# Optimization experiments

Hardware: AMD Instinct MI355X
Metric: run time of the kernel (lower is better)

The kernel has to match this reference:

```python
import jax, jax.numpy as jnp
import numpy as np

N, E, H, HEADS, L = 10000, 64000, 128, 8, 8
D = H // HEADS
CUTOFF = 5.0
EPS = 1e-5


def _xavier(key, shape):
    lim = float(np.sqrt(6.0 / (shape[0] + shape[1])))
    return jax.random.uniform(key, shape, minval=-lim, maxval=lim, dtype=jnp.float32)


def setup_inputs() -> dict:
    key = jax.random.key(0)
    ks = jax.random.split(key, 20)
    zeros = lambda *s: jnp.zeros(s, jnp.float32)
    return {
        "x": jax.random.normal(ks[0], (N, H), jnp.float32),
        "vec": 0.1 * jax.random.normal(ks[1], (N, L, H), jnp.float32),
        "f_ij": jax.random.normal(ks[2], (E, H), jnp.float32),
        "d_ij": jax.random.normal(ks[3], (E, L), jnp.float32),
        "r_ij": jax.random.uniform(ks[4], (E,), jnp.float32, 0.0, CUTOFF),
        "edge_index": jax.random.randint(ks[5], (2, E), 0, N),
        "ln_g": jnp.ones((H,), jnp.float32), "ln_b": zeros(H),
        "vln_w": jnp.ones((H,), jnp.float32),
        "W_vec": _xavier(ks[6], (H, 3 * H)),
        "W_q": _xavier(ks[7], (H, H)), "b_q": zeros(H),
        "W_k": _xavier(ks[8], (H, H)), "b_k": zeros(H),
        "W_v": _xavier(ks[9], (H, H)), "b_v": zeros(H),
        "W_dk": _xavier(ks[10], (H, H)), "b_dk": zeros(H),
        "W_dv": _xavier(ks[11], (H, H)), "b_dv": zeros(H),
        "W_s": _xavier(ks[12], (H, 2 * H)), "b_s": zeros(2 * H),
        "W_f": _xavier(ks[13], (H, H)), "b_f": zeros(H),
        "W_src": _xavier(ks[14], (H, H)),
        "W_trg": _xavier(ks[15], (H, H)),
        "W_o": _xavier(ks[16], (H, 3 * H)), "b_o": zeros(3 * H),
    }


def _layernorm(x, g, b):
    mu = jnp.mean(x, -1, keepdims=True)
    var = jnp.mean((x - mu) ** 2, -1, keepdims=True)
    return (x - mu) * jax.lax.rsqrt(var + EPS) * g + b


def _cutoff(r):
    # CosineCutoff: 0.5*(cos(pi*r/cutoff)+1) for r < cutoff
    return 0.5 * (jnp.cos(jnp.pi * r / CUTOFF) + 1.0) * (r < CUTOFF).astype(r.dtype)


def _vec_rejection(v, d):
    # v: [E, L, H], d: [E, L]; remove the component of v along d (per channel)
    proj = jnp.einsum("elh,el->eh", v, d)
    return v - proj[:, None, :] * d[:, :, None]


def reference(x, vec, f_ij, d_ij, r_ij, edge_index, ln_g, ln_b, vln_w, W_vec,
              W_q, b_q, W_k, b_k, W_v, b_v, W_dk, b_dk, W_dv, b_dv,
              W_s, b_s, W_f, b_f, W_src, W_trg, W_o, b_o):
    src, dst = edge_index[0], edge_index[1]  # j (source), i (target)
    x = _layernorm(x, ln_g, ln_b)
    vec = vec * vln_w  # VecLayerNorm with norm_type="none": identity norm * weight

    q = (x @ W_q + b_q).reshape(N, HEADS, D)
    k = (x @ W_k + b_k).reshape(N, HEADS, D)
    v = (x @ W_v + b_v).reshape(N, HEADS, D)
    dk = jax.nn.silu(f_ij @ W_dk + b_dk).reshape(E, HEADS, D)
    dv = jax.nn.silu(f_ij @ W_dv + b_dv).reshape(E, HEADS, D)

    vec1, vec2, vec3 = jnp.split(jnp.einsum("nlh,hk->nlk", vec, W_vec), 3, axis=-1)
    vec_dot = jnp.sum(vec1 * vec2, axis=1)  # [N, H]

    # ---- message (per edge) ----
    attn = jnp.sum(q[dst] * k[src] * dk, axis=-1)          # [E, HEADS]
    attn = jax.nn.silu(attn) * _cutoff(r_ij)[:, None]
    vm = (v[src] * dv * attn[:, :, None]).reshape(E, H)    # [E, H]
    s1, s2 = jnp.split(jax.nn.silu(vm @ W_s + b_s), 2, axis=-1)
    vec_m = vec[src] * s1[:, None, :] + s2[:, None, :] * d_ij[:, :, None]  # [E, L, H]

    # ---- aggregate (scatter-add to target nodes) ----
    x_agg = jax.ops.segment_sum(vm, dst, num_segments=N)       # [N, H]
    vec_agg = jax.ops.segment_sum(vec_m, dst, num_segments=N)  # [N, L, H]

    # ---- edge update ----
    w1 = _vec_rejection(jnp.einsum("elh,hk->elk", vec[dst], W_trg), d_ij)
    w2 = _vec_rejection(jnp.einsum("elh,hk->elk", vec[src], W_src), -d_ij)
    w_dot = jnp.sum(w1 * w2, axis=1)                       # [E, H]
    df_ij = jax.nn.silu(f_ij @ W_f + b_f) * w_dot

    # ---- node update ----
    o1, o2, o3 = jnp.split(x_agg @ W_o + b_o, 3, axis=-1)
    dx = vec_dot * o2 + o3
    dvec = vec3 * o1[:, None, :] + vec_agg
    return dx, dvec, df_ij
```

## Files before the change

kernel.cpp:

```cpp
#include <hip/hip_runtime.h>
#include <hip/hip_bf16.h>
#include <math.h>

#define N_NODES 10000
#define N_EDGES 64000
#define H 128
#define L 8
#define NL (N_NODES * L)

typedef __attribute__((ext_vector_type(4))) float f32x4;
typedef __attribute__((ext_vector_type(8))) __bf16 bf16x8;
typedef __attribute__((ext_vector_type(4))) __bf16 bf16x4;

__device__ __forceinline__ float silu_f(float x) { return x / (1.f + __expf(-x)); }

__global__ __launch_bounds__(256) void ln_kernel(const float* __restrict__ x,
                                                 const float* __restrict__ g,
                                                 const float* __restrict__ b,
                                                 __bf16* __restrict__ out, int n_nodes) {
  int wave = threadIdx.x >> 6;
  int lane = threadIdx.x & 63;
  int n = blockIdx.x * 4 + wave;
  if (n >= n_nodes) return;
  const float* xr = x + (size_t)n * H;
  float a0 = xr[lane], a1 = xr[lane + 64];
  float s = a0 + a1;
#pragma unroll
  for (int off = 32; off >= 1; off >>= 1) s += __shfl_xor(s, off, 64);
  float mu = s * (1.f / H);
  float d0 = a0 - mu, d1 = a1 - mu;
  float v = d0 * d0 + d1 * d1;
#pragma unroll
  for (int off = 32; off >= 1; off >>= 1) v += __shfl_xor(v, off, 64);
  float rstd = rsqrtf(v * (1.f / H) + 1e-5f);
  __bf16* orow = out + (size_t)n * H;
  orow[lane] = (__bf16)(d0 * rstd * g[lane] + b[lane]);
  orow[lane + 64] = (__bf16)(d1 * rstd * g[lane + 64] + b[lane + 64]);
}

__global__ __launch_bounds__(256) void vecw_kernel(const float* __restrict__ vec,
                                                   const float* __restrict__ w,
                                                   __bf16* __restrict__ out,
                                                   __bf16* __restrict__ vv) {
  int n = blockIdx.x * 2 + (threadIdx.x >> 7);
  int h = threadIdx.x & 127;
  float wl = w[h];
  const float* base = vec + (size_t)n * 1024 + h;
  __bf16* orow = out + (size_t)n * 1024 + h;
  bf16x8 pack;
#pragma unroll
  for (int l = 0; l < 8; ++l) {
    __bf16 bv = (__bf16)(base[l * 128] * wl);
    orow[l * 128] = bv;
    pack[l] = bv;
  }
  *(bf16x8*)(vv + (size_t)n * 2048 + h * 16) = pack;
}

__global__ __launch_bounds__(256) void gatherf2b_kernel(const float* __restrict__ in,
                                                        const int* __restrict__ elist,
                                                        __bf16* __restrict__ out) {
  int p = blockIdx.x * 8 + (threadIdx.x >> 5);
  int c = (threadIdx.x & 31) * 4;
  int e = elist[p];
  f32x4 a = *(const f32x4*)(in + (size_t)e * 128 + c);
  bf16x4 h;
  h[0] = (__bf16)a[0]; h[1] = (__bf16)a[1]; h[2] = (__bf16)a[2]; h[3] = (__bf16)a[3];
  *(bf16x4*)(out + (size_t)p * 128 + c) = h;
}

__global__ __launch_bounds__(256) void wconv_kernel(
    const float* __restrict__ Wvec, const float* __restrict__ Wq, const float* __restrict__ Wk,
    const float* __restrict__ Wv, const float* __restrict__ Wdk, const float* __restrict__ Wdv,
    const float* __restrict__ Ws, const float* __restrict__ Wtrg, const float* __restrict__ Wsrc,
    const float* __restrict__ Wf, const float* __restrict__ Wo,
    const float* __restrict__ bq, const float* __restrict__ bk, const float* __restrict__ bv,
    const float* __restrict__ bdk, const float* __restrict__ bdv, const float* __restrict__ bf,
    __bf16* __restrict__ Wt, float* __restrict__ bqkv, float* __restrict__ bfm) {
  int bid = blockIdx.x;
  int t = threadIdx.x;
  if (bid >= 256) {
    if (bid == 256) {
      if (t < 128) { bqkv[t] = bq[t]; bqkv[128 + t] = bk[t]; bqkv[256 + t] = bv[t]; }
    } else {
      if (t < 128) { bfm[t] = bdk[t]; bfm[128 + t] = bdv[t]; bfm[256 + t] = bf[t]; }
    }
    return;
  }
  int ct = bid >> 2, kt = bid & 3;
  int gc0 = ct * 32;
  const float* W; int ldw, sc0;
  if      (gc0 < 384)  { W = Wvec; ldw = 384; sc0 = gc0; }
  else if (gc0 < 512)  { W = Wtrg; ldw = 128; sc0 = gc0 - 384; }
  else if (gc0 < 640)  { W = Wsrc; ldw = 128; sc0 = gc0 - 512; }
  else if (gc0 < 768)  { W = Wq;   ldw = 128; sc0 = gc0 - 640; }
  else if (gc0 < 896)  { W = Wk;   ldw = 128; sc0 = gc0 - 768; }
  else if (gc0 < 1024) { W = Wv;   ldw = 128; sc0 = gc0 - 896; }
  else if (gc0 < 1152) { W = Wdk;  ldw = 128; sc0 = gc0 - 1024; }
  else if (gc0 < 1280) { W = Wdv;  ldw = 128; sc0 = gc0 - 1152; }
  else if (gc0 < 1408) { W = Wf;   ldw = 128; sc0 = gc0 - 1280; }
  else if (gc0 < 1664) { W = Ws;   ldw = 256; sc0 = gc0 - 1408; }
  else                 { W = Wo;   ldw = 384; sc0 = gc0 - 1664; }
  __shared__ float tile[32][33];
  int tx = t & 31, ty = t >> 5;
#pragma unroll
  for (int i = 0; i < 4; ++i)
    tile[ty + i * 8][tx] = W[(size_t)(kt * 32 + ty + i * 8) * ldw + sc0 + tx];
  __syncthreads();
#pragma unroll
  for (int i = 0; i < 4; ++i)
    Wt[(size_t)(gc0 + ty + i * 8) * 128 + kt * 32 + tx] = (__bf16)tile[tx][ty + i * 8];
}

__global__ __launch_bounds__(256, 2) void vdot_gemm(const __bf16* __restrict__ A,
                                                    const __bf16* __restrict__ Bt,
                                                    float* __restrict__ vdot) {
  __shared__ __bf16 As[128 * 128];
  const int tid = threadIdx.x;
  const int lane = tid & 63;
  const int wave = tid >> 6;
  const int wm = wave >> 1, wn = wave & 1;
  const int row0 = blockIdx.x * 128;

#pragma unroll
  for (int i = 0; i < 8; ++i) {
    int c = tid + i * 256;
    int row = c >> 4, k8 = c & 15;
    int k8s = k8 ^ (row & 7);
    const __bf16* src = A + (size_t)(row0 + row) * 128 + k8s * 8;
    __builtin_amdgcn_global_load_lds((const __attribute__((address_space(1))) void*)src,
                                     (__attribute__((address_space(3))) void*)(As + c * 8),
                                     16, 0, 0);
  }
  __syncthreads();

  f32x4 pacc[4][4], acc[4][4];
#pragma unroll
  for (int mi = 0; mi < 4; ++mi)
#pragma unroll
    for (int ni = 0; ni < 4; ++ni) {
      pacc[mi][ni] = f32x4{0.f, 0.f, 0.f, 0.f};
      acc[mi][ni] = f32x4{0.f, 0.f, 0.f, 0.f};
    }
#pragma unroll
  for (int ct = 0; ct < 2; ++ct) {
    const __bf16* Bbase =
        Bt + ((size_t)(ct * 128 + wn * 64 + (lane & 15)) << 7) + ((lane >> 4) << 3);
#pragma unroll
    for (int ks = 0; ks < 4; ++ks) {
      bf16x8 b[4];
#pragma unroll
      for (int ni = 0; ni < 4; ++ni) b[ni] = *(const bf16x8*)(Bbase + (ni << 11) + (ks << 5));
      bf16x8 a[4];
#pragma unroll
      for (int mi = 0; mi < 4; ++mi) {
        int row = wm * 64 + mi * 16 + (lane & 15);
        int byte = (row * 256 + ks * 64 + ((lane >> 4) << 4)) ^ ((row & 7) << 4);
        a[mi] = *(const bf16x8*)((const char*)As + byte);
      }
      if (ct == 0) {
#pragma unroll
        for (int mi = 0; mi < 4; ++mi)
#pragma unroll
          for (int ni = 0; ni < 4; ++ni)
            pacc[mi][ni] =
                __builtin_amdgcn_mfma_f32_16x16x32_bf16(a[mi], b[ni], pacc[mi][ni], 0, 0, 0);
      } else {
#pragma unroll
        for (int mi = 0; mi < 4; ++mi)
#pragma unroll
          for (int ni = 0; ni < 4; ++ni)
            acc[mi][ni] =
                __builtin_amdgcn_mfma_f32_16x16x32_bf16(a[mi], b[ni], acc[mi][ni], 0, 0, 0);
      }
    }
  }
#pragma unroll
  for (int mi = 0; mi < 4; ++mi) {
#pragma unroll
    for (int ni = 0; ni < 4; ++ni) {
      float sr = pacc[mi][ni][0] * acc[mi][ni][0] + pacc[mi][ni][1] * acc[mi][ni][1] +
                 pacc[mi][ni][2] * acc[mi][ni][2] + pacc[mi][ni][3] * acc[mi][ni][3];
      sr += __shfl_xor(sr, 16, 64);
      if ((lane & 16) == 0) {
        int node = (row0 >> 3) + wm * 8 + mi * 2 + (lane >> 5);
        int col = wn * 64 + ni * 16 + (lane & 15);
        vdot[(size_t)node * 128 + col] = sr;
      }
    }
  }
}

template <typename CT>
__global__ __launch_bounds__(256, 3) void gemm_v9(const __bf16* __restrict__ A,
                                                  const __bf16* __restrict__ Bt,
                                                  const float* __restrict__ bias,
                                                  CT* __restrict__ C, int M, int nx, int ny,
                                                  int ldc, int act) {
  __shared__ __bf16 As[128 * 128];
  __bf16* Cs = As;
  const int bid = blockIdx.x;
  const int xi = bid & 7;
  const int rem = bid >> 3;
  const int y = rem % ny;
  const int x = (rem / ny) * 8 + xi;
  if (x >= nx) return;
  const int tid = threadIdx.x;
  const int lane = tid & 63;
  const int wave = tid >> 6;
  const int wm = wave >> 1, wn = wave & 1;
  const int row0 = x * 128;

#pragma unroll
  for (int i = 0; i < 8; ++i) {
    int c = tid + i * 256;
    int row = c >> 4, k8 = c & 15;
    int k8s = k8 ^ (row & 7);
    const __bf16* src = A + (size_t)(row0 + row) * 128 + k8s * 8;
    __builtin_amdgcn_global_load_lds((const __attribute__((address_space(1))) void*)src,
                                     (__attribute__((address_space(3))) void*)(As + c * 8),
                                     16, 0, 0);
  }
  __syncthreads();

  const __bf16* Bbase =
      Bt + ((size_t)(y * 128 + wn * 64 + (lane & 15)) << 7) + ((lane >> 4) << 3);
  bf16x8 b[4][4];
#pragma unroll
  for (int ks = 0; ks < 4; ++ks)
#pragma unroll
    for (int ni = 0; ni < 4; ++ni) b[ks][ni] = *(const bf16x8*)(Bbase + (ni << 11) + (ks << 5));

  f32x4 acc[4][4];
#pragma unroll
  for (int mi = 0; mi < 4; ++mi)
#pragma unroll
    for (int ni = 0; ni < 4; ++ni) acc[mi][ni] = f32x4{0.f, 0.f, 0.f, 0.f};

#pragma unroll
  for (int ks = 0; ks < 4; ++ks) {
    bf16x8 a[4];
#pragma unroll
    for (int mi = 0; mi < 4; ++mi) {
      int row = wm * 64 + mi * 16 + (lane & 15);
      int byte = (row * 256 + ks * 64 + ((lane >> 4) << 4)) ^ ((row & 7) << 4);
      a[mi] = *(const bf16x8*)((const char*)As + byte);
    }
#pragma unroll
    for (int mi = 0; mi < 4; ++mi)
#pragma unroll
      for (int ni = 0; ni < 4; ++ni)
        acc[mi][ni] =
            __builtin_amdgcn_mfma_f32_16x16x32_bf16(a[mi], b[ks][ni], acc[mi][ni], 0, 0, 0);
  }

  const int cstore = y * 128;
  if constexpr (sizeof(CT) == 2) {
#pragma unroll
    for (int p = 0; p < 2; ++p) {
      __syncthreads();
      int rl = (wm << 5) | ((lane >> 4) << 2);
#pragma unroll
      for (int q = 0; q < 2; ++q) {
        int mi = 2 * p + q;
#pragma unroll
        for (int ni = 0; ni < 4; ++ni) {
          int col = wn * 64 + ni * 16 + (lane & 15);
          float bv = bias ? bias[cstore + col] : 0.f;
#pragma unroll
          for (int r = 0; r < 4; ++r) {
            float xv = acc[mi][ni][r] + bv;
            if (act) xv = silu_f(xv);
            Cs[(rl + q * 16 + r) * 136 + col] = (__bf16)xv;
          }
        }
      }
      __syncthreads();
#pragma unroll
      for (int rr = 0; rr < 4; ++rr) {
        int row = (tid >> 4) + rr * 16;
        int chunk = tid & 15;
        bf16x8 v = *(const bf16x8*)(Cs + row * 136 + chunk * 8);
        int grow = row0 + (row >> 5) * 64 + (2 * p + ((row >> 4) & 1)) * 16 + (row & 15);
        if (grow < M)
          *(bf16x8*)(C + (size_t)grow * ldc + cstore + chunk * 8) = v;
      }
    }
  } else {
#pragma unroll
    for (int mi = 0; mi < 4; ++mi) {
      int rbase = row0 + wm * 64 + mi * 16 + ((lane >> 4) << 2);
#pragma unroll
      for (int ni = 0; ni < 4; ++ni) {
        int gcol = cstore + wn * 64 + ni * 16 + (lane & 15);
        float bv = bias ? bias[cstore + wn * 64 + ni * 16 + (lane & 15)] : 0.f;
#pragma unroll
        for (int r = 0; r < 4; ++r) {
          int grow = rbase + r;
          if (grow < M) {
            float xv = acc[mi][ni][r] + bv;
            if (act) xv = silu_f(xv);
            C[(size_t)grow * ldc + gcol] = (CT)xv;
          }
        }
      }
    }
  }
}

__global__ __launch_bounds__(256, 3) void gemm_big(const __bf16* __restrict__ A,
                                                   const __bf16* __restrict__ Bt,
                                                   __bf16* __restrict__ vec3,
                                                   __bf16* __restrict__ vtT,
                                                   __bf16* __restrict__ vv, int nx) {
  __shared__ __bf16 As[128 * 128];
  __bf16* Cs = As;
  const int bid = blockIdx.x;
  const int xi = bid & 7;
  const int rem = bid >> 3;
  const int y = rem % 3;
  const int x = (rem / 3) * 8 + xi;
  if (x >= nx) return;
  const int tid = threadIdx.x;
  const int lane = tid & 63;
  const int wave = tid >> 6;
  const int wm = wave >> 1, wn = wave & 1;
  const int row0 = x * 128;

#pragma unroll
  for (int i = 0; i < 8; ++i) {
    int c = tid + i * 256;
    int row = c >> 4, k8 = c & 15;
    int k8s = k8 ^ (row & 7);
    const __bf16* src = A + (size_t)(row0 + row) * 128 + k8s * 8;
    __builtin_amdgcn_global_load_lds((const __attribute__((address_space(1))) void*)src,
                                     (__attribute__((address_space(3))) void*)(As + c * 8),
                                     16, 0, 0);
  }
  __syncthreads();

  const __bf16* Bbase =
      Bt + ((size_t)(y * 128 + wn * 64 + (lane & 15)) << 7) + ((lane >> 4) << 3);
  bf16x8 b[4][4];
#pragma unroll
  for (int ks = 0; ks < 4; ++ks)
#pragma unroll
    for (int ni = 0; ni < 4; ++ni) b[ks][ni] = *(const bf16x8*)(Bbase + (ni << 11) + (ks << 5));

  f32x4 acc[4][4];
#pragma unroll
  for (int mi = 0; mi < 4; ++mi)
#pragma unroll
    for (int ni = 0; ni < 4; ++ni) acc[mi][ni] = f32x4{0.f, 0.f, 0.f, 0.f};

#pragma unroll
  for (int ks = 0; ks < 4; ++ks) {
    bf16x8 a[4];
#pragma unroll
    for (int mi = 0; mi < 4; ++mi) {
      int row = wm * 64 + mi * 16 + (lane & 15);
      int byte = (row * 256 + ks * 64 + ((lane >> 4) << 4)) ^ ((row & 7) << 4);
      a[mi] = *(const bf16x8*)((const char*)As + byte);
    }
#pragma unroll
    for (int mi = 0; mi < 4; ++mi)
#pragma unroll
      for (int ni = 0; ni < 4; ++ni)
        acc[mi][ni] =
            __builtin_amdgcn_mfma_f32_16x16x32_bf16(a[mi], b[ks][ni], acc[mi][ni], 0, 0, 0);
  }

  __bf16* T = (y == 1) ? vtT : vv;
  const int hs = (y == 1) ? 8 : 16;
  const int off = (y == 1) ? 0 : 8;
  const size_t rstride = (y == 1) ? 1024 : 2048;
#pragma unroll
  for (int p = 0; p < 2; ++p) {
    __syncthreads();
    int rl = (wm << 5) | ((lane >> 4) << 2);
#pragma unroll
    for (int q = 0; q < 2; ++q) {
      int mi = 2 * p + q;
#pragma unroll
      for (int ni = 0; ni < 4; ++ni) {
        int col = wn * 64 + ni * 16 + (lane & 15);
#pragma unroll
        for (int r = 0; r < 4; ++r)
          Cs[(rl + q * 16 + r) * 136 + col] = (__bf16)acc[mi][ni][r];
      }
    }
    __syncthreads();
    if (y == 0) {
#pragma unroll
      for (int rr = 0; rr < 4; ++rr) {
        int row = (tid >> 4) + rr * 16;
        int chunk = tid & 15;
        bf16x8 v = *(const bf16x8*)(Cs + row * 136 + chunk * 8);
        int grow = row0 + (row >> 5) * 64 + (2 * p + ((row >> 4) & 1)) * 16 + (row & 15);
        *(bf16x8*)(vec3 + (size_t)grow * 128 + chunk * 8) = v;
      }
    } else {
#pragma unroll
      for (int j = 0; j < 4; ++j) {
        int idx = tid + 256 * j;
        int node_idx = idx >> 7;
        int h = idx & 127;
        int wmm = node_idx >> 2, qq = (node_idx >> 1) & 1, w = node_idx & 1;
        int base = wmm * 32 + qq * 16 + w * 8;
        bf16x8 v;
#pragma unroll
        for (int l = 0; l < 8; ++l) v[l] = Cs[(base + l) * 136 + h];
        int g = (row0 >> 3) + wmm * 8 + (2 * p + qq) * 2 + w;
        *(bf16x8*)(T + (size_t)g * rstride + h * hs + off) = v;
      }
    }
  }
}

static inline int swz_grid(int nx, int ny) { return ((nx + 7) / 8) * ny * 8; }

__global__ __launch_bounds__(256) void msg_kernel(const __bf16* __restrict__ qkv,
                                                  const __bf16* __restrict__ fm,
                                                  const float* __restrict__ r_ij,
                                                  const int* __restrict__ ei,
                                                  const int* __restrict__ elist,
                                                  __bf16* __restrict__ vm) {
  int p = blockIdx.x * 2 + (threadIdx.x >> 7);
  int h = threadIdx.x & 127;
  int e = elist[p];
  int src = ei[e], dst = ei[N_EDGES + e];
  float qv = (float)qkv[(size_t)dst * 384 + h];
  float kv = (float)qkv[(size_t)src * 384 + 128 + h];
  float vv = (float)qkv[(size_t)src * 384 + 256 + h];
  float t = qv * kv * (float)fm[(size_t)p * 384 + h];
#pragma unroll
  for (int off = 8; off >= 1; off >>= 1) t += __shfl_xor(t, off, 16);
  float r = r_ij[e];
  float cut = 0.5f * (__cosf(0.6283185307f * r) + 1.f);
  cut = (r < 5.f) ? cut : 0.f;
  float attn = silu_f(t) * cut;
  vm[(size_t)p * H + h] = (__bf16)(vv * (float)fm[(size_t)p * 384 + 128 + h] * attn);
}

__global__ __launch_bounds__(256) void hist_kernel(const int* __restrict__ ei,
                                                   int* __restrict__ cnt) {
  int e = blockIdx.x * 256 + threadIdx.x;
  if (e < N_EDGES) atomicAdd(&cnt[ei[N_EDGES + e]], 1);
}

__global__ __launch_bounds__(1024) void scan_kernel(const int* __restrict__ cnt,
                                                    int* __restrict__ rowptr) {
  __shared__ int wsum[16];
  int t = threadIdx.x;
  int base = t * 10;
  int local[10];
  int s = 0;
#pragma unroll
  for (int i = 0; i < 10; ++i) {
    int v = (base + i < N_NODES) ? cnt[base + i] : 0;
    local[i] = s;
    s += v;
  }
  int lane = t & 63, wave = t >> 6;
  int inc = s;
#pragma unroll
  for (int off = 1; off < 64; off <<= 1) {
    int u = __shfl_up(inc, off, 64);
    if (lane >= off) inc += u;
  }
  if (lane == 63) wsum[wave] = inc;
  __syncthreads();
  if (t == 0) {
    int acc = 0;
#pragma unroll
    for (int w = 0; w < 16; ++w) { int v = wsum[w]; wsum[w] = acc; acc += v; }
  }
  __syncthreads();
  int excl = inc - s + wsum[wave];
#pragma unroll
  for (int i = 0; i < 10; ++i)
    if (base + i <= N_NODES) rowptr[base + i] = excl + local[i];
}

__global__ __launch_bounds__(256) void fill_kernel(const int* __restrict__ ei,
                                                   const int* __restrict__ rowptr,
                                                   int* __restrict__ cursor,
                                                   int* __restrict__ elist) {
  int e = blockIdx.x * 256 + threadIdx.x;
  if (e < N_EDGES) {
    int d = ei[N_EDGES + e];
    int p = atomicAdd(&cursor[d], 1);
    elist[rowptr[d] + p] = e;
  }
}

__global__ __launch_bounds__(256) void node_kernel(const __bf16* __restrict__ vm,
                                                   const __bf16* __restrict__ s,
                                                   const __bf16* __restrict__ vv,
                                                   const __bf16* __restrict__ vtT,
                                                   const __bf16* __restrict__ fm,
                                                   const float* __restrict__ d_ij,
                                                   const int* __restrict__ ei,
                                                   const int* __restrict__ rowptr,
                                                   const int* __restrict__ elist,
                                                   __bf16* __restrict__ x_agg,
                                                   float* __restrict__ dvec,
                                                   float* __restrict__ df) {
  int n = blockIdx.x * 2 + (threadIdx.x >> 7);
  int h = threadIdx.x & 127;
  if (n >= N_NODES) return;
  int beg = rowptr[n], end = rowptr[n + 1];

  bf16x8 vt8 = *(const bf16x8*)(vtT + (size_t)n * 1024 + h * 8);
  float vt[L];
#pragma unroll
  for (int l = 0; l < L; l++) vt[l] = (float)vt8[l];

  float ax = 0.f;
  float av[L] = {};
  for (int p = beg; p < end; ++p) {
    int e = elist[p];
    int src = ei[e];
    const float* dd = d_ij + (size_t)e * L;
    float d[L], sd2 = 0.f;
#pragma unroll
    for (int l = 0; l < L; l++) {
      d[l] = dd[l];
      sd2 += d[l] * d[l];
    }
    ax += (float)vm[(size_t)p * H + h];
    float s1 = (float)s[(size_t)p * 256 + h];
    float s2 = (float)s[(size_t)p * 256 + 128 + h];
    const __bf16* vbase = vv + (size_t)src * 2048 + h * 16;
    bf16x8 vw8 = *(const bf16x8*)(vbase);
    bf16x8 vs8 = *(const bf16x8*)(vbase + 8);
    float dot = 0.f, p1 = 0.f, p2 = 0.f;
#pragma unroll
    for (int l = 0; l < L; l++) {
      av[l] += (float)vw8[l] * s1 + s2 * d[l];
      float bb = (float)vs8[l];
      dot += vt[l] * bb;
      p1 += vt[l] * d[l];
      p2 += bb * d[l];
    }
    float wdot = dot - p1 * p2 * (2.f - sd2);
    df[(size_t)e * H + h] = (float)fm[(size_t)p * 384 + 256 + h] * wdot;
  }
  x_agg[(size_t)n * H + h] = (__bf16)ax;
  float* drow = dvec + (size_t)n * L * H + h;
#pragma unroll
  for (int l = 0; l < L; l++) drow[l * H] = av[l];
}

__global__ __launch_bounds__(256) void final_kernel(const float* __restrict__ o,
                                                    const float* __restrict__ vdot,
                                                    const __bf16* __restrict__ vec3,
                                                    float* __restrict__ dx,
                                                    float* __restrict__ dvec, int n_nodes) {
  int n = blockIdx.x * 2 + (threadIdx.x >> 7);
  int h = threadIdx.x & 127;
  if (n >= n_nodes) return;
  float o1 = o[(size_t)n * 384 + h];
  float o2 = o[(size_t)n * 384 + 128 + h];
  float o3 = o[(size_t)n * 384 + 256 + h];
  dx[(size_t)n * H + h] = vdot[(size_t)n * H + h] * o2 + o3;
  float* drow = dvec + (size_t)n * L * H + h;
  const __bf16* v3 = vec3 + (size_t)n * 1024 + h;
#pragma unroll
  for (int l = 0; l < L; l++) drow[l * H] += (float)v3[l * 128] * o1;
}

extern "C" void kernel_launch(void* const* d_in, const int* in_sizes, int n_in, void* d_out,
                              int out_size, void* d_ws, size_t ws_size, hipStream_t stream) {
  const float* x = (const float*)d_in[0];
  const float* vec = (const float*)d_in[1];
  const float* f_ij = (const float*)d_in[2];
  const float* d_ij = (const float*)d_in[3];
  const float* r_ij = (const float*)d_in[4];
  const int* ei = (const int*)d_in[5];
  const float* ln_g = (const float*)d_in[6];
  const float* ln_b = (const float*)d_in[7];
  const float* vln_w = (const float*)d_in[8];
  const float* W_vec = (const float*)d_in[9];
  const float* W_q = (const float*)d_in[10];
  const float* b_q = (const float*)d_in[11];
  const float* W_k = (const float*)d_in[12];
  const float* b_k = (const float*)d_in[13];
  const float* W_v = (const float*)d_in[14];
  const float* b_v = (const float*)d_in[15];
  const float* W_dk = (const float*)d_in[16];
  const float* b_dk = (const float*)d_in[17];
  const float* W_dv = (const float*)d_in[18];
  const float* b_dv = (const float*)d_in[19];
  const float* W_s = (const float*)d_in[20];
  const float* b_s = (const float*)d_in[21];
  const float* W_f = (const float*)d_in[22];
  const float* b_f = (const float*)d_in[23];
  const float* W_src = (const float*)d_in[24];
  const float* W_trg = (const float*)d_in[25];
  const float* W_o = (const float*)d_in[26];
  const float* b_o = (const float*)d_in[27];

  float* out = (float*)d_out;
  float* dx = out;
  float* dvec = out + (size_t)N_NODES * H;
  float* df = dvec + (size_t)N_NODES * L * H;

  float* ws = (float*)d_ws;
  __bf16* vecw = (__bf16*)ws;
  __bf16* vec3 = (__bf16*)(ws + 5120000);
  __bf16* vtT = (__bf16*)(ws + 10240000);
  __bf16* fm = (__bf16*)(ws + 20480000);
  __bf16* vm = (__bf16*)(ws + 32768000);
  __bf16* s_buf = (__bf16*)(ws + 36864000);
  __bf16* qkv = (__bf16*)(ws + 45056000);
  __bf16* xln = (__bf16*)(ws + 48896000);
  __bf16* xagg = (__bf16*)(ws + 49536000);
  float* vdot = ws + 50176000;
  __bf16* Wt = (__bf16*)(ws + 51456000);
  float* bqkv = ws + 51456000 + 131072;
  float* bfm = bqkv + 384;
  int* rowptr = (int*)(bfm + 384);
  int* elist = rowptr + 10001;
  int* cnt = elist + 64000;
  int* cursor = cnt + 10000;
  __bf16* fijb = (__bf16*)(ws + 51800000);
  __bf16* vv = (__bf16*)(ws + 56000000);

  float* o_buf = ws + 45056000;

  dim3 b256(256);

  hipMemsetAsync(cnt, 0, N_NODES * sizeof(int), stream);
  hipMemsetAsync(cursor, 0, N_NODES * sizeof(int), stream);
  hist_kernel<<<dim3((N_EDGES + 255) / 256), b256, 0, stream>>>(ei, cnt);
  scan_kernel<<<dim3(1), dim3(1024), 0, stream>>>(cnt, rowptr);
  fill_kernel<<<dim3((N_EDGES + 255) / 256), b256, 0, stream>>>(ei, rowptr, cursor, elist);

  wconv_kernel<<<dim3(258), b256, 0, stream>>>(W_vec, W_q, W_k, W_v, W_dk, W_dv, W_s, W_trg,
                                               W_src, W_f, W_o, b_q, b_k, b_v, b_dk, b_dv, b_f,
                                               Wt, bqkv, bfm);
  gatherf2b_kernel<<<dim3(N_EDGES / 8), b256, 0, stream>>>(f_ij, elist, fijb);
  ln_kernel<<<dim3((N_NODES + 3) / 4), b256, 0, stream>>>(x, ln_g, ln_b, xln, N_NODES);
  vecw_kernel<<<dim3(N_NODES / 2), b256, 0, stream>>>(vec, vln_w, vecw, vv);
  vdot_gemm<<<dim3(625), b256, 0, stream>>>(vecw, Wt, vdot);
  gemm_big<<<dim3(swz_grid(625, 3)), b256, 0, stream>>>(vecw, Wt + (size_t)256 * 128, vec3,
                                                        vtT, vv, 625);
  gemm_v9<__bf16><<<dim3(swz_grid(79, 3)), b256, 0, stream>>>(
      xln, Wt + (size_t)640 * 128, bqkv, qkv, N_NODES, 79, 3, 384, 0);
  gemm_v9<__bf16><<<dim3(swz_grid(500, 3)), b256, 0, stream>>>(
      fijb, Wt + (size_t)1024 * 128, bfm, fm, N_EDGES, 500, 3, 384, 1);
  msg_kernel<<<dim3(N_EDGES / 2), b256, 0, stream>>>(qkv, fm, r_ij, ei, elist, vm);
  gemm_v9<__bf16><<<dim3(swz_grid(500, 2)), b256, 0, stream>>>(
      vm, Wt + (size_t)1408 * 128, b_s, s_buf, N_EDGES, 500, 2, 256, 1);
  node_kernel<<<dim3(N_NODES / 2), b256, 0, stream>>>(vm, s_buf, vv, vtT, fm, d_ij, ei,
                                                      rowptr, elist, xagg, dvec, df);
  gemm_v9<float><<<dim3(swz_grid(79, 3)), b256, 0, stream>>>(
      xagg, Wt + (size_t)1664 * 128, b_o, o_buf, N_NODES, 79, 3, 384, 0);
  final_kernel<<<dim3(5000), b256, 0, stream>>>(o_buf, vdot, vec3, dx, dvec, N_NODES);
}
```

Baseline: 323.5 us.

## Presort edge indices and d/r by destination, split vv into separate buffers, prefetch in node loop

Fill now also writes src and dst lists in CSR order, and a new gather kernel copies d_ij and r_ij into sorted order. msg and node kernels then read contiguous per-position data and avoid the elist-to-edge_index double indirection. The interleaved vv buffer is split into separate vecwT and vsT arrays. The node loop software-prefetches the next source's vectors. This adds one extra small gather kernel and more workspace, in exchange for fewer dependent random loads in the per-edge hot loops.

After: 320.8 us. Within noise of the previous version (-0.8%).

```diff
diff --git a/kernel.cpp b/kernel.cpp
--- a/kernel.cpp
+++ b/kernel.cpp
@@ -41,7 +41,7 @@
 __global__ __launch_bounds__(256) void vecw_kernel(const float* __restrict__ vec,
                                                    const float* __restrict__ w,
                                                    __bf16* __restrict__ out,
-                                                   __bf16* __restrict__ vv) {
+                                                   __bf16* __restrict__ vecwT) {
   int n = blockIdx.x * 2 + (threadIdx.x >> 7);
   int h = threadIdx.x & 127;
   float wl = w[h];
@@ -54,7 +54,7 @@
     orow[l * 128] = bv;
     pack[l] = bv;
   }
-  *(bf16x8*)(vv + (size_t)n * 2048 + h * 16) = pack;
+  *(bf16x8*)(vecwT + (size_t)n * 1024 + h * 8) = pack;
 }
 
 __global__ __launch_bounds__(256) void gatherf2b_kernel(const float* __restrict__ in,
@@ -67,6 +67,18 @@
   bf16x4 h;
   h[0] = (__bf16)a[0]; h[1] = (__bf16)a[1]; h[2] = (__bf16)a[2]; h[3] = (__bf16)a[3];
   *(bf16x4*)(out + (size_t)p * 128 + c) = h;
+}
+
+__global__ __launch_bounds__(256) void dgather_kernel(const float* __restrict__ d_ij,
+                                                      const float* __restrict__ r_ij,
+                                                      const int* __restrict__ elist,
+                                                      float* __restrict__ d2,
+                                                      float* __restrict__ r2) {
+  int idx = blockIdx.x * 256 + threadIdx.x;
+  int p = idx >> 3, j = idx & 7;
+  int e = elist[p];
+  d2[idx] = d_ij[(size_t)e * 8 + j];
+  if (j == 0) r2[p] = r_ij[e];
 }
 
 __global__ __launch_bounds__(256) void wconv_kernel(
@@ -312,7 +324,7 @@
                                                    const __bf16* __restrict__ Bt,
                                                    __bf16* __restrict__ vec3,
                                                    __bf16* __restrict__ vtT,
-                                                   __bf16* __restrict__ vv, int nx) {
+                                                   __bf16* __restrict__ vsT, int nx) {
   __shared__ __bf16 As[128 * 128];
   __bf16* Cs = As;
   const int bid = blockIdx.x;
@@ -370,10 +382,7 @@
             __builtin_amdgcn_mfma_f32_16x16x32_bf16(a[mi], b[ks][ni], acc[mi][ni], 0, 0, 0);
   }
 
-  __bf16* T = (y == 1) ? vtT : vv;
-  const int hs = (y == 1) ? 8 : 16;
-  const int off = (y == 1) ? 0 : 8;
-  const size_t rstride = (y == 1) ? 1024 : 2048;
+  __bf16* T = (y == 1) ? vtT : vsT;
 #pragma unroll
   for (int p = 0; p < 2; ++p) {
     __syncthreads();
@@ -411,7 +420,7 @@
 #pragma unroll
         for (int l = 0; l < 8; ++l) v[l] = Cs[(base + l) * 136 + h];
         int g = (row0 >> 3) + wmm * 8 + (2 * p + qq) * 2 + w;
-        *(bf16x8*)(T + (size_t)g * rstride + h * hs + off) = v;
+        *(bf16x8*)(T + (size_t)g * 1024 + h * 8) = v;
       }
     }
   }
@@ -421,21 +430,20 @@
 
 __global__ __launch_bounds__(256) void msg_kernel(const __bf16* __restrict__ qkv,
                                                   const __bf16* __restrict__ fm,
-                                                  const float* __restrict__ r_ij,
-                                                  const int* __restrict__ ei,
-                                                  const int* __restrict__ elist,
+                                                  const float* __restrict__ r2,
+                                                  const int* __restrict__ srclist,
+                                                  const int* __restrict__ dstlist,
                                                   __bf16* __restrict__ vm) {
   int p = blockIdx.x * 2 + (threadIdx.x >> 7);
   int h = threadIdx.x & 127;
-  int e = elist[p];
-  int src = ei[e], dst = ei[N_EDGES + e];
+  int src = srclist[p], dst = dstlist[p];
   float qv = (float)qkv[(size_t)dst * 384 + h];
   float kv = (float)qkv[(size_t)src * 384 + 128 + h];
   float vv = (float)qkv[(size_t)src * 384 + 256 + h];
   float t = qv * kv * (float)fm[(size_t)p * 384 + h];
 #pragma unroll
   for (int off = 8; off >= 1; off >>= 1) t += __shfl_xor(t, off, 16);
-  float r = r_ij[e];
+  float r = r2[p];
   float cut = 0.5f * (__cosf(0.6283185307f * r) + 1.f);
   cut = (r < 5.f) ? cut : 0.f;
   float attn = silu_f(t) * cut;
@@ -485,24 +493,31 @@
 __global__ __launch_bounds__(256) void fill_kernel(const int* __restrict__ ei,
                                                    const int* __restrict__ rowptr,
                                                    int* __restrict__ cursor,
-                                                   int* __restrict__ elist) {
+                                                   int* __restrict__ elist,
+                                                   int* __restrict__ srclist,
+                                                   int* __restrict__ dstlist) {
   int e = blockIdx.x * 256 + threadIdx.x;
   if (e < N_EDGES) {
+    int s = ei[e];
     int d = ei[N_EDGES + e];
     int p = atomicAdd(&cursor[d], 1);
-    elist[rowptr[d] + p] = e;
+    int idx = rowptr[d] + p;
+    elist[idx] = e;
+    srclist[idx] = s;
+    dstlist[idx] = d;
   }
 }
 
 __global__ __launch_bounds__(256) void node_kernel(const __bf16* __restrict__ vm,
                                                    const __bf16* __restrict__ s,
-                                                   const __bf16* __restrict__ vv,
+                                                   const __bf16* __restrict__ vecwT,
                                                    const __bf16* __restrict__ vtT,
+                                                   const __bf16* __restrict__ vsT,
                                                    const __bf16* __restrict__ fm,
-                                                   const float* __restrict__ d_ij,
-                                                   const int* __restrict__ ei,
+                                                   const float* __restrict__ d2,
+                                                   const int* __restrict__ srclist,
+                                                   const int* __restrict__ elist,
                                                    const int* __restrict__ rowptr,
-                                                   const int* __restrict__ elist,
                                                    __bf16* __restrict__ x_agg,
                                                    float* __restrict__ dvec,
                                                    float* __restrict__ df) {
@@ -518,33 +533,41 @@
 
   float ax = 0.f;
   float av[L] = {};
-  for (int p = beg; p < end; ++p) {
-    int e = elist[p];
-    int src = ei[e];
-    const float* dd = d_ij + (size_t)e * L;
-    float d[L], sd2 = 0.f;
-#pragma unroll
-    for (int l = 0; l < L; l++) {
-      d[l] = dd[l];
-      sd2 += d[l] * d[l];
-    }
-    ax += (float)vm[(size_t)p * H + h];
-    float s1 = (float)s[(size_t)p * 256 + h];
-    float s2 = (float)s[(size_t)p * 256 + 128 + h];
-    const __bf16* vbase = vv + (size_t)src * 2048 + h * 16;
-    bf16x8 vw8 = *(const bf16x8*)(vbase);
-    bf16x8 vs8 = *(const bf16x8*)(vbase + 8);
-    float dot = 0.f, p1 = 0.f, p2 = 0.f;
-#pragma unroll
-    for (int l = 0; l < L; l++) {
-      av[l] += (float)vw8[l] * s1 + s2 * d[l];
-      float bb = (float)vs8[l];
-      dot += vt[l] * bb;
-      p1 += vt[l] * d[l];
-      p2 += bb * d[l];
-    }
-    float wdot = dot - p1 * p2 * (2.f - sd2);
-    df[(size_t)e * H + h] = (float)fm[(size_t)p * 384 + 256 + h] * wdot;
+  if (beg < end) {
+    int src = srclist[beg];
+    bf16x8 vw8 = *(const bf16x8*)(vecwT + (size_t)src * 1024 + h * 8);
+    bf16x8 vs8 = *(const bf16x8*)(vsT + (size_t)src * 1024 + h * 8);
+    for (int p = beg; p < end; ++p) {
+      bf16x8 vw_n = {}, vs_n = {};
+      if (p + 1 < end) {
+        int sn = srclist[p + 1];
+        vw_n = *(const bf16x8*)(vecwT + (size_t)sn * 1024 + h * 8);
+        vs_n = *(const bf16x8*)(vsT + (size_t)sn * 1024 + h * 8);
+      }
+      const float* dd = d2 + (size_t)p * L;
+      float d[L], sd2 = 0.f;
+#pragma unroll
+      for (int l = 0; l < L; l++) {
+        d[l] = dd[l];
+        sd2 += d[l] * d[l];
+      }
+      ax += (float)vm[(size_t)p * H + h];
+      float s1 = (float)s[(size_t)p * 256 + h];
+      float s2 = (float)s[(size_t)p * 256 + 128 + h];
+      float dot = 0.f, p1 = 0.f, p2 = 0.f;
+#pragma unroll
+      for (int l = 0; l < L; l++) {
+        av[l] += (float)vw8[l] * s1 + s2 * d[l];
+        float bb = (float)vs8[l];
+        dot += vt[l] * bb;
+        p1 += vt[l] * d[l];
+        p2 += bb * d[l];
+      }
+      float wdot = dot - p1 * p2 * (2.f - sd2);
+      df[(size_t)elist[p] * H + h] = (float)fm[(size_t)p * 384 + 256 + h] * wdot;
+      vw8 = vw_n;
+      vs8 = vs_n;
+    }
   }
   x_agg[(size_t)n * H + h] = (__bf16)ax;
   float* drow = dvec + (size_t)n * L * H + h;
@@ -610,6 +633,7 @@
   __bf16* vecw = (__bf16*)ws;
   __bf16* vec3 = (__bf16*)(ws + 5120000);
   __bf16* vtT = (__bf16*)(ws + 10240000);
+  __bf16* vsT = (__bf16*)(ws + 15360000);
   __bf16* fm = (__bf16*)(ws + 20480000);
   __bf16* vm = (__bf16*)(ws + 32768000);
   __bf16* s_buf = (__bf16*)(ws + 36864000);
@@ -622,10 +646,14 @@
   float* bfm = bqkv + 384;
   int* rowptr = (int*)(bfm + 384);
   int* elist = rowptr + 10001;
-  int* cnt = elist + 64000;
+  int* srclist = elist + 64000;
+  int* dstlist = srclist + 64000;
+  int* cnt = dstlist + 64000;
   int* cursor = cnt + 10000;
-  __bf16* fijb = (__bf16*)(ws + 51800000);
-  __bf16* vv = (__bf16*)(ws + 56000000);
+  __bf16* fijb = (__bf16*)(ws + 51900000);
+  __bf16* vecwT = (__bf16*)(ws + 56000000);
+  float* d2 = ws + 61200000;
+  float* r2 = ws + 61712000;
 
   float* o_buf = ws + 45056000;
 
@@ -635,26 +663,28 @@
   hipMemsetAsync(cursor, 0, N_NODES * sizeof(int), stream);
   hist_kernel<<<dim3((N_EDGES + 255) / 256), b256, 0, stream>>>(ei, cnt);
   scan_kernel<<<dim3(1), dim3(1024), 0, stream>>>(cnt, rowptr);
-  fill_kernel<<<dim3((N_EDGES + 255) / 256), b256, 0, stream>>>(ei, rowptr, cursor, elist);
+  fill_kernel<<<dim3((N_EDGES + 255) / 256), b256, 0, stream>>>(ei, rowptr, cursor, elist,
+                                                                srclist, dstlist);
+  dgather_kernel<<<dim3(N_EDGES * 8 / 256), b256, 0, stream>>>(d_ij, r_ij, elist, d2, r2);
+  gatherf2b_kernel<<<dim3(N_EDGES / 8), b256, 0, stream>>>(f_ij, elist, fijb);
 
   wconv_kernel<<<dim3(258), b256, 0, stream>>>(W_vec, W_q, W_k, W_v, W_dk, W_dv, W_s, W_trg,
                                                W_src, W_f, W_o, b_q, b_k, b_v, b_dk, b_dv, b_f,
                                                Wt, bqkv, bfm);
-  gatherf2b_kernel<<<dim3(N_EDGES / 8), b256, 0, stream>>>(f_ij, elist, fijb);
   ln_kernel<<<dim3((N_NODES + 3) / 4), b256, 0, stream>>>(x, ln_g, ln_b, xln, N_NODES);
-  vecw_kernel<<<dim3(N_NODES / 2), b256, 0, stream>>>(vec, vln_w, vecw, vv);
+  vecw_kernel<<<dim3(N_NODES / 2), b256, 0, stream>>>(vec, vln_w, vecw, vecwT);
   vdot_gemm<<<dim3(625), b256, 0, stream>>>(vecw, Wt, vdot);
   gemm_big<<<dim3(swz_grid(625, 3)), b256, 0, stream>>>(vecw, Wt + (size_t)256 * 128, vec3,
-                                                        vtT, vv, 625);
+                                                        vtT, vsT, 625);
   gemm_v9<__bf16><<<dim3(swz_grid(79, 3)), b256, 0, stream>>>(
       xln, Wt + (size_t)640 * 128, bqkv, qkv, N_NODES, 79, 3, 384, 0);
   gemm_v9<__bf16><<<dim3(swz_grid(500, 3)), b256, 0, stream>>>(
       fijb, Wt + (size_t)1024 * 128, bfm, fm, N_EDGES, 500, 3, 384, 1);
-  msg_kernel<<<dim3(N_EDGES / 2), b256, 0, stream>>>(qkv, fm, r_ij, ei, elist, vm);
+  msg_kernel<<<dim3(N_EDGES / 2), b256, 0, stream>>>(qkv, fm, r2, srclist, dstlist, vm);
   gemm_v9<__bf16><<<dim3(swz_grid(500, 2)), b256, 0, stream>>>(
       vm, Wt + (size_t)1408 * 128, b_s, s_buf, N_EDGES, 500, 2, 256, 1);
-  node_kernel<<<dim3(N_NODES / 2), b256, 0, stream>>>(vm, s_buf, vv, vtT, fm, d_ij, ei,
-                                                      rowptr, elist, xagg, dvec, df);
+  node_kernel<<<dim3(N_NODES / 2), b256, 0, stream>>>(vm, s_buf, vecwT, vtT, vsT, fm, d2,
+                                                      srclist, elist, rowptr, xagg, dvec, df);
   gemm_v9<float><<<dim3(swz_grid(79, 3)), b256, 0, stream>>>(
       xagg, Wt + (size_t)1664 * 128, b_o, o_buf, N_NODES, 79, 3, 384, 0);
   final_kernel<<<dim3(5000), b256, 0, stream>>>(o_buf, vdot, vec3, dx, dvec, N_NODES);
```
